# Optimization experiments

Measured on AMD Instinct MI355X. Metric: run time of the kernel, lower is better.

Reference implementation:

```python
import jax, jax.numpy as jnp
import numpy as np

B, L, D = 4, 2048, 512
H = 8
DH = D // H  # 64
SCALE = DH // H  # faithful to source: key.size(-1)//num_heads = 64//8 = 8 (multiplicative)
LN_EPS = 1e-5


def setup_inputs() -> dict:
    key = jax.random.key(0)
    ks = jax.random.split(key, 16)
    s = 1.0 / np.sqrt(D)
    inp = {
        "query": jax.random.normal(ks[0], (B, L, D), jnp.float32),
        "key": jax.random.normal(ks[1], (B, L, D), jnp.float32),
        "value": jax.random.normal(ks[2], (B, L, D), jnp.float32),
        "Wq": jax.random.uniform(ks[3], (D, D), jnp.float32, -s, s),
        "bq": jax.random.uniform(ks[4], (D,), jnp.float32, -s, s),
        "Wk": jax.random.uniform(ks[5], (D, D), jnp.float32, -s, s),
        "bk": jax.random.uniform(ks[6], (D,), jnp.float32, -s, s),
        "Wv": jax.random.uniform(ks[7], (D, D), jnp.float32, -s, s),
        "bv": jax.random.uniform(ks[8], (D,), jnp.float32, -s, s),
        "Wo": jax.random.uniform(ks[9], (D, D), jnp.float32, -s, s),
        "bo": jax.random.uniform(ks[10], (D,), jnp.float32, -s, s),
        "gamma": jnp.ones((D,), jnp.float32),
        "beta": jnp.zeros((D,), jnp.float32),
    }
    return inp


def _layer_norm(x, gamma, beta):
    mu = jnp.mean(x, axis=-1, keepdims=True)
    var = jnp.mean(jnp.square(x - mu), axis=-1, keepdims=True)
    return (x - mu) * jax.lax.rsqrt(var + LN_EPS) * gamma + beta


def reference(query, key, value, Wq, bq, Wk, bk, Wv, bv, Wo, bo, gamma, beta):
    res = query
    # QKV projections: [B, L, D]
    q = query @ Wq.T + bq
    k = key @ Wk.T + bk
    v = value @ Wv.T + bv
    # faithful to source: raw view(B*H, -1, DH) with NO transpose
    q = q.reshape(B * H, -1, DH)
    k = k.reshape(B * H, -1, DH)
    v = v.reshape(B * H, -1, DH)
    # bmm -> multiplicative scale -> softmax(dim=2) -> bmm
    attn = jnp.einsum('bqd,bkd->bqk', q, k) * SCALE  # [B*H, L, L]
    attn = jax.nn.softmax(attn, axis=2)
    ctx = jnp.einsum('bqk,bkd->bqd', attn, v)        # [B*H, L, DH]
    ctx = ctx.reshape(B, -1, DH * H)                  # [B, L, D]
    out = ctx @ Wo.T + bo
    out = _layer_norm(res + out, gamma, beta)
    return (out, attn)
```

## Files before the change

### kernel.cpp

```cpp
#include <hip/hip_runtime.h>

#define LSEQ 2048
#define DMODEL 512
#define DHD 64
#define SLAB (LSEQ*DHD)

typedef __attribute__((ext_vector_type(8))) short short8;
typedef __attribute__((ext_vector_type(4))) short short4v;
typedef __attribute__((ext_vector_type(4))) float f32x4;
typedef float f4raw __attribute__((ext_vector_type(4)));
typedef _Float16 half8 __attribute__((ext_vector_type(8)));
typedef _Float16 h4_t  __attribute__((ext_vector_type(4)));

__device__ __forceinline__ short f2bf(float x) {
    union { float f; unsigned u; } v; v.f = x;
    unsigned r = v.u + 0x7FFF + ((v.u >> 16) & 1);
    return (short)(r >> 16);
}
__device__ __forceinline__ float bf2f(short h) {
    union { float f; unsigned u; } v; v.u = ((unsigned)(unsigned short)h) << 16;
    return v.f;
}

#define GLOAD_LDS16(g, l) __builtin_amdgcn_global_load_lds( \
    (const __attribute__((address_space(1))) void*)(g),     \
    (__attribute__((address_space(3))) void*)(l), 16, 0, 0)

#define VMCNT0()  asm volatile("s_waitcnt vmcnt(0)" ::: "memory")
#define VMCNT2()  asm volatile("s_waitcnt vmcnt(2)" ::: "memory")
#define VMCNT4()  asm volatile("s_waitcnt vmcnt(4)" ::: "memory")
#define LGKM0()   asm volatile("s_waitcnt lgkmcnt(0)" ::: "memory")
#define SCHEDB()  __builtin_amdgcn_sched_barrier(0)
#define BARRIER() do { __builtin_amdgcn_s_barrier(); __builtin_amdgcn_sched_barrier(0); } while (0)

__global__ __launch_bounds__(256) void convw_kernel(
    const float* __restrict__ W0, const float* __restrict__ W1,
    const float* __restrict__ W2, const float* __restrict__ W3,
    short* __restrict__ F0, short* __restrict__ F1,
    short* __restrict__ F2, short* __restrict__ F3)
{
    const int which = blockIdx.y;
    const float* W = which==0 ? W0 : which==1 ? W1 : which==2 ? W2 : W3;
    short*       F = which==0 ? F0 : which==1 ? F1 : which==2 ? F2 : F3;

    const int g  = blockIdx.x * 256 + threadIdx.x;
    const int n  = g >> 6, kc = g & 63;
    const float* src = W + (size_t)n * 512 + kc * 8;
    float4 a0 = *(const float4*)src;
    float4 a1 = *(const float4*)(src + 4);
    float v[8] = {a0.x,a0.y,a0.z,a0.w,a1.x,a1.y,a1.z,a1.w};
    short8 h, l;
    #pragma unroll
    for (int j = 0; j < 8; ++j) { short hh = f2bf(v[j]); h[j] = hh; l[j] = f2bf(v[j] - bf2f(hh)); }

    const int nt = n >> 4, fr = n & 15, kt = kc >> 2, kg = kc & 3;
    short* dh = F + ((size_t)(nt*16 + kt) * 2) * 512 + fr*32 + kg*8;
    *(short8*)dh        = h;
    *(short8*)(dh + 512) = l;
}

template<int MODE>
__global__ __launch_bounds__(512) void proj2_kernel(
    const float* __restrict__ A0, const float* __restrict__ A1, const float* __restrict__ A2,
    const short* __restrict__ F0, const short* __restrict__ F1, const short* __restrict__ F2,
    const float* __restrict__ b0, const float* __restrict__ b1, const float* __restrict__ b2,
    float* __restrict__ Cf0, float* __restrict__ Cf1, float* __restrict__ Cf2,
    short* __restrict__ C00, short* __restrict__ C01, short* __restrict__ C02)
{
    __shared__ __align__(16) short Ah[64][40], Al[64][40];

    const int z = blockIdx.z;
    const float* A    = z==0 ? A0 : z==1 ? A1 : A2;
    const short* F    = z==0 ? F0 : z==1 ? F1 : F2;
    const float* bias = z==0 ? b0 : z==1 ? b1 : b2;
    float* Cf         = z==0 ? Cf0 : z==1 ? Cf1 : Cf2;
    short* C0         = z==0 ? C00 : z==1 ? C01 : C02;

    const int tid  = threadIdx.x;
    const int lane = tid & 63, wv = tid >> 6;
    const int fr = lane & 15, kg = lane >> 4;
    const int m0 = blockIdx.y * 64, n0 = blockIdx.x * 256;

    f32x4 acc[4][2];
    #pragma unroll
    for (int i = 0; i < 4; ++i)
        #pragma unroll
        for (int j = 0; j < 2; ++j) { f32x4 zo = {0.f,0.f,0.f,0.f}; acc[i][j] = zo; }

    const int srow = tid >> 3, sc4 = (tid & 7) << 2;

    for (int kt = 0; kt < 16; ++kt) {
        __syncthreads();
        {
            const float* ap = A + (size_t)(m0 + srow) * DMODEL + kt*32 + sc4;
            float4 a0 = *(const float4*)ap;
            float v[4] = {a0.x, a0.y, a0.z, a0.w};
            short4v h, l;
            #pragma unroll
            for (int j = 0; j < 4; ++j) { short hh = f2bf(v[j]); h[j] = hh; l[j] = f2bf(v[j] - bf2f(hh)); }
            *(short4v*)&Ah[srow][sc4] = h;
            *(short4v*)&Al[srow][sc4] = l;
        }
        __syncthreads();

        short8 ah[4], al[4];
        #pragma unroll
        for (int mf = 0; mf < 4; ++mf) {
            ah[mf] = *(short8*)&Ah[mf*16 + fr][kg*8];
            al[mf] = *(short8*)&Al[mf*16 + fr][kg*8];
        }
        #pragma unroll
        for (int nf = 0; nf < 2; ++nf) {
            const int nt = (n0 >> 4) + wv*2 + nf;
            const short* wf = F + ((size_t)(nt*16 + kt) * 2) * 512 + fr*32 + kg*8;
            short8 wh = *(const short8*)wf;
            short8 wl = *(const short8*)(wf + 512);
            #pragma unroll
            for (int mf = 0; mf < 4; ++mf) {
                acc[mf][nf] = __builtin_amdgcn_mfma_f32_16x16x32_bf16(ah[mf], wh, acc[mf][nf], 0,0,0);
                acc[mf][nf] = __builtin_amdgcn_mfma_f32_16x16x32_bf16(ah[mf], wl, acc[mf][nf], 0,0,0);
                acc[mf][nf] = __builtin_amdgcn_mfma_f32_16x16x32_bf16(al[mf], wh, acc[mf][nf], 0,0,0);
            }
        }
    }

    #pragma unroll
    for (int nf = 0; nf < 2; ++nf) {
        const int col = n0 + wv*32 + nf*16 + fr;
        const float bv = bias[col];
        #pragma unroll
        for (int mf = 0; mf < 4; ++mf) {
            #pragma unroll
            for (int r = 0; r < 4; ++r) {
                const int row = m0 + mf*16 + kg*4 + r;
                const float o = acc[mf][nf][r] + bv;
                const size_t idx = (size_t)row * DMODEL + col;
                if (MODE == 0) Cf[idx] = o;
                else           ((_Float16*)C0)[idx] = (_Float16)o;
            }
        }
    }
}

__global__ __launch_bounds__(256) void vtransf_kernel(
    const short* __restrict__ vh, short* __restrict__ vtf)
{
    __shared__ short T[64][72];
    const int tid = threadIdx.x;
    const int s  = blockIdx.y;
    const int t0 = blockIdx.x * 64;
    const size_t slab = (size_t)s * SLAB;

    {
        const int r = tid >> 2, c0 = (tid & 3) << 4;
        const short* src = vh + slab + (size_t)(t0 + r) * DHD + c0;
        short8 a = *(const short8*)src;
        short8 b = *(const short8*)(src + 8);
        *(short8*)&T[r][c0]     = a;
        *(short8*)&T[r][c0 + 8] = b;
    }
    __syncthreads();
    {
        const int kbl = tid >> 6, d = tid & 63;
        short8 o0, o1;
        #pragma unroll
        for (int j = 0; j < 8; ++j) { o0[j] = T[kbl*16 + j][d]; o1[j] = T[kbl*16 + 8 + j][d]; }
        short* dst = vtf + slab + ((size_t)((t0 >> 4) + kbl) * 64 + d) * 16;
        *(short8*)dst       = o0;
        *(short8*)(dst + 8) = o1;
    }
}

__global__ __launch_bounds__(512, 4) void attn_kernel(
    const _Float16* __restrict__ qf, const _Float16* __restrict__ kf,
    const _Float16* __restrict__ vtf,
    float* __restrict__ attn, float* __restrict__ ctx)
{
    __shared__ __align__(16) char KBuf[49152];
    __shared__ float redA[8][16];
    __shared__ float mrow[16], lirow[16];

    const int tid  = threadIdx.x;
    const int lane = tid & 63, wv = tid >> 6;
    const int fr = lane & 15, kg = lane >> 4;

    const int wg  = blockIdx.x;
    const int rem = wg & 1023;
    const int q0  = (rem >> 3) << 4;
    const int bh  = ((wg >> 10) << 3) + (rem & 7);
    const size_t slab = (size_t)bh * SLAB;

    half8 qa[2];
    #pragma unroll
    for (int ks = 0; ks < 2; ++ks)
        qa[ks] = *(const half8*)(qf + slab + (size_t)(q0 + fr) * DHD + ks*32 + kg*8);

    const int srow = lane >> 3;
    const int scb  = (lane & 7) ^ srow;

    f32x4 s[16];

    #define STAGE_K(TI, CUR) { \
        _Pragma("unroll") \
        for (int j = 0; j < 2; ++j) { \
            const int b = wv*2 + j; \
            GLOAD_LDS16(kf + slab + (size_t)((TI)*128 + b*8 + srow)*DHD + scb*8, \
                        KBuf + (CUR)*16384 + b*1024); \
        } }

    STAGE_K(0, 0);
    STAGE_K(1, 1);

    const int klo = (wv << 4) + fr;
    const int sw  = fr & 7;
    #pragma unroll
    for (int i = 0; i < 16; ++i) {
        if (i + 2 < 16) {
            SCHEDB();
            LGKM0();
            STAGE_K(i + 2, (i + 2) % 3);
        }

        if      (i <= 13) VMCNT4();
        else if (i == 14) VMCNT2();
        else              VMCNT0();

        const char* rp = KBuf + (i % 3)*16384 + (klo << 7);
        half8 kb0 = *(const half8*)(rp + ((kg ^ sw) << 4));
        half8 kb1 = *(const half8*)(rp + (((4 + kg) ^ sw) << 4));

        f32x4 a = {0.f,0.f,0.f,0.f};
        a = __builtin_amdgcn_mfma_f32_16x16x32_f16(kb0, qa[0], a, 0,0,0);
        a = __builtin_amdgcn_mfma_f32_16x16x32_f16(kb1, qa[1], a, 0,0,0);
        s[i] = a;
    }
    #undef STAGE_K

    float m;
    {
        f32x4 mx = s[0];
        #pragma unroll
        for (int i = 1; i < 16; ++i) {
            mx.x = fmaxf(mx.x, s[i].x); mx.y = fmaxf(mx.y, s[i].y);
            mx.z = fmaxf(mx.z, s[i].z); mx.w = fmaxf(mx.w, s[i].w);
        }
        m = fmaxf(fmaxf(mx.x, mx.y), fmaxf(mx.z, mx.w));
        m = fmaxf(m, __shfl_xor(m, 16));
        m = fmaxf(m, __shfl_xor(m, 32));
    }
    if (lane < 16) redA[wv][lane] = m;
    __syncthreads();
    if (tid < 16) {
        float mm = redA[0][tid];
        #pragma unroll
        for (int w = 1; w < 8; ++w) mm = fmaxf(mm, redA[w][tid]);
        mrow[tid] = mm;
    }
    __syncthreads();
    m = mrow[fr];

    const float C = 8.0f * 1.44269504089f;
    float sum = 0.f;
    #pragma unroll
    for (int i = 0; i < 16; ++i) {
        f32x4 p;
        p.x = exp2f((s[i].x - m) * C);
        p.y = exp2f((s[i].y - m) * C);
        p.z = exp2f((s[i].z - m) * C);
        p.w = exp2f((s[i].w - m) * C);
        s[i] = p;
        sum += (p.x + p.y) + (p.z + p.w);
    }
    sum += __shfl_xor(sum, 16);
    sum += __shfl_xor(sum, 32);
    if (lane < 16) redA[wv][lane] = sum;
    __syncthreads();
    if (tid < 16) {
        float l = 0.f;
        #pragma unroll
        for (int w = 0; w < 8; ++w) l += redA[w][tid];
        lirow[tid] = 1.0f / l;
    }
    __syncthreads();
    const float li = lirow[fr];

    f32x4 acc[4];
    #pragma unroll
    for (int db = 0; db < 4; ++db) { f32x4 z = {0.f,0.f,0.f,0.f}; acc[db] = z; }

    _Float16* PBh = (_Float16*)KBuf;
    const _Float16* vfb = vtf + slab;
    const int sq = tid >> 5, sc = tid & 31;
    float* abase = attn + ((size_t)bh * LSEQ + q0 + sq) * LSEQ + (sc << 2);

    int cur = 0;
    #pragma unroll
    for (int t = 0; t < 16; ++t) {
        f32x4 p = s[t];
        p.x *= li; p.y *= li; p.z *= li; p.w *= li;
        h4_t pw = { (_Float16)p.x, (_Float16)p.y, (_Float16)p.z, (_Float16)p.w };

        *(h4_t*)&PBh[(size_t)cur*2176 + fr*136 + (wv << 4) + (kg << 2)] = pw;

        const _Float16* vb = vfb + ((size_t)(t*8 + wv) << 10) + (fr << 4) + (kg << 2);
        #pragma unroll
        for (int db = 0; db < 4; ++db) {
            h4_t va = *(const h4_t*)(vb + db*256);
            acc[db] = __builtin_amdgcn_mfma_f32_16x16x16f16(va, pw, acc[db], 0,0,0);
        }

        LGKM0();
        BARRIER();

        h4_t pr = *(const h4_t*)&PBh[(size_t)cur*2176 + sq*136 + (sc << 2)];
        f4raw o = { (float)pr[0], (float)pr[1], (float)pr[2], (float)pr[3] };
        __builtin_nontemporal_store(o, (f4raw*)(abase + (size_t)t * 128));

        cur ^= 1;
    }

    __syncthreads();
    {
        float* pt = (float*)KBuf;
        #pragma unroll
        for (int db = 0; db < 4; ++db) {
            float4 o = { acc[db].x, acc[db].y, acc[db].z, acc[db].w };
            *(float4*)(pt + wv*1024 + fr*64 + db*16 + (kg << 2)) = o;
        }
    }
    __syncthreads();
    {
        float* pt = (float*)KBuf;
        const int e = tid << 1;
        const int q = e >> 6, d = e & 63;
        float2 r2 = {0.f, 0.f};
        #pragma unroll
        for (int w = 0; w < 8; ++w) {
            float2 t2 = *(float2*)(pt + w*1024 + q*64 + d);
            r2.x += t2.x; r2.y += t2.y;
        }
        *(float2*)(ctx + slab + (size_t)(q0 + q) * DHD + d) = r2;
    }
}

__global__ __launch_bounds__(128) void ln_kernel(
    const float* __restrict__ resid, const float* __restrict__ x,
    const float* __restrict__ gamma, const float* __restrict__ beta,
    float* __restrict__ out)
{
    const int row = blockIdx.x;
    const int tid = threadIdx.x;
    const size_t base = (size_t)row * DMODEL + tid*4;

    float4 v = *(const float4*)(x + base);
    float4 rq = *(const float4*)(resid + base);
    v.x += rq.x; v.y += rq.y; v.z += rq.z; v.w += rq.w;

    float s  = v.x + v.y + v.z + v.w;
    float ss = v.x*v.x + v.y*v.y + v.z*v.z + v.w*v.w;
    #pragma unroll
    for (int d = 1; d < 64; d <<= 1) { s += __shfl_xor(s, d); ss += __shfl_xor(ss, d); }

    __shared__ float red[2][2];
    const int wv = tid >> 6;
    if ((tid & 63) == 0) { red[wv][0] = s; red[wv][1] = ss; }
    __syncthreads();
    s  = red[0][0] + red[1][0];
    ss = red[0][1] + red[1][1];

    const float mu  = s * (1.0f/512.0f);
    const float var = ss * (1.0f/512.0f) - mu*mu;
    const float rs  = rsqrtf(var + 1e-5f);

    float4 g = *(const float4*)(gamma + tid*4);
    float4 b = *(const float4*)(beta + tid*4);
    float4 o;
    o.x = (v.x - mu) * rs * g.x + b.x;
    o.y = (v.y - mu) * rs * g.y + b.y;
    o.z = (v.z - mu) * rs * g.z + b.z;
    o.w = (v.w - mu) * rs * g.w + b.w;
    *(float4*)(out + base) = o;
}

extern "C" void kernel_launch(void* const* d_in, const int* in_sizes, int n_in,
                              void* d_out, int out_size, void* d_ws, size_t ws_size,
                              hipStream_t stream)
{
    const float* query = (const float*)d_in[0];
    const float* key   = (const float*)d_in[1];
    const float* value = (const float*)d_in[2];
    const float* Wq = (const float*)d_in[3];
    const float* bq = (const float*)d_in[4];
    const float* Wk = (const float*)d_in[5];
    const float* bk = (const float*)d_in[6];
    const float* Wv = (const float*)d_in[7];
    const float* bv = (const float*)d_in[8];
    const float* Wo = (const float*)d_in[9];
    const float* bo = (const float*)d_in[10];
    const float* gamma = (const float*)d_in[11];
    const float* beta  = (const float*)d_in[12];

    float* out  = (float*)d_out;
    float* attn = out + 4194304;

    const size_t NTOK = (size_t)8192 * 512;
    short* qv = (short*)d_ws;
    short* kv = qv + NTOK;
    short* vf = kv + NTOK;
    short* vtf = vf + NTOK;
    short* wfq = vtf + NTOK;
    short* wfk = wfq + 524288;
    short* wfv = wfk + 524288;
    short* wfo = wfv + 524288;
    float* obuf = (float*)d_ws;

    convw_kernel<<<dim3(128, 4), 256, 0, stream>>>(Wq, Wk, Wv, Wo, wfq, wfk, wfv, wfo);

    proj2_kernel<3><<<dim3(2, 128, 3), 512, 0, stream>>>(
        query, key, value, wfq, wfk, wfv, bq, bk, bv,
        nullptr, nullptr, nullptr, qv, kv, vf);

    vtransf_kernel<<<dim3(32, 32), 256, 0, stream>>>(vf, vtf);

    attn_kernel<<<4096, 512, 0, stream>>>((const _Float16*)qv, (const _Float16*)kv,
                                          (const _Float16*)vtf, attn, out );

    proj2_kernel<0><<<dim3(2, 128, 1), 512, 0, stream>>>(
        out , out, out, wfo, wfo, wfo, bo, bo, bo,
        obuf, obuf, obuf, nullptr, nullptr, nullptr);

    ln_kernel<<<8192, 128, 0, stream>>>(query, obuf, gamma, beta, out);
}
```

Before: 248.7 us.

## Fuse V transpose into QKV projection and LayerNorm into output projection

The QKV projection epilogue now writes V directly in the transposed tiled layout the attention kernel expects, removing the separate transpose kernel and its round trip. The output projection is rewritten so each block owns 64 full rows and applies bias, residual add and LayerNorm in its epilogue, removing the intermediate fp32 buffer and the separate LN kernel. The trade-off is that the output projection now launches only 128 blocks, giving low GPU occupancy, and the V stores become scattered 2-byte writes.

```diff
diff --git a/kernel.cpp b/kernel.cpp
--- a/kernel.cpp
+++ b/kernel.cpp
@@ -59,13 +59,11 @@
     *(short8*)(dh + 512) = l;
 }
 
-template<int MODE>
-__global__ __launch_bounds__(512) void proj2_kernel(
+__global__ __launch_bounds__(512) void projqkv_kernel(
     const float* __restrict__ A0, const float* __restrict__ A1, const float* __restrict__ A2,
     const short* __restrict__ F0, const short* __restrict__ F1, const short* __restrict__ F2,
     const float* __restrict__ b0, const float* __restrict__ b1, const float* __restrict__ b2,
-    float* __restrict__ Cf0, float* __restrict__ Cf1, float* __restrict__ Cf2,
-    short* __restrict__ C00, short* __restrict__ C01, short* __restrict__ C02)
+    short* __restrict__ qv, short* __restrict__ kv, short* __restrict__ vtf)
 {
     __shared__ __align__(16) short Ah[64][40], Al[64][40];
 
@@ -73,8 +71,6 @@
     const float* A    = z==0 ? A0 : z==1 ? A1 : A2;
     const short* F    = z==0 ? F0 : z==1 ? F1 : F2;
     const float* bias = z==0 ? b0 : z==1 ? b1 : b2;
-    float* Cf         = z==0 ? Cf0 : z==1 ? Cf1 : Cf2;
-    short* C0         = z==0 ? C00 : z==1 ? C01 : C02;
 
     const int tid  = threadIdx.x;
     const int lane = tid & 63, wv = tid >> 6;
@@ -133,41 +129,132 @@
             #pragma unroll
             for (int r = 0; r < 4; ++r) {
                 const int row = m0 + mf*16 + kg*4 + r;
-                const float o = acc[mf][nf][r] + bv;
-                const size_t idx = (size_t)row * DMODEL + col;
-                if (MODE == 0) Cf[idx] = o;
-                else           ((_Float16*)C0)[idx] = (_Float16)o;
-            }
-        }
-    }
-}
-
-__global__ __launch_bounds__(256) void vtransf_kernel(
-    const short* __restrict__ vh, short* __restrict__ vtf)
+                const _Float16 o = (_Float16)(acc[mf][nf][r] + bv);
+                if (z == 2) {
+                    const int s_ = row >> 8;
+                    const int l_ = ((row & 255) << 3) | (col >> 6);
+                    const int d_ = col & 63;
+                    ((_Float16*)vtf)[(size_t)s_*SLAB + (((l_ >> 4)*64 + d_) << 4) + (l_ & 15)] = o;
+                } else {
+                    _Float16* C = (z == 0) ? (_Float16*)qv : (_Float16*)kv;
+                    C[(size_t)row * DMODEL + col] = o;
+                }
+            }
+        }
+    }
+}
+
+__global__ __launch_bounds__(512) void proj3_kernel(
+    const float* __restrict__ A, const short* __restrict__ F,
+    const float* __restrict__ bias, const float* __restrict__ resid,
+    const float* __restrict__ gamma, const float* __restrict__ beta,
+    float* __restrict__ out)
 {
-    __shared__ short T[64][72];
-    const int tid = threadIdx.x;
-    const int s  = blockIdx.y;
-    const int t0 = blockIdx.x * 64;
-    const size_t slab = (size_t)s * SLAB;
-
-    {
-        const int r = tid >> 2, c0 = (tid & 3) << 4;
-        const short* src = vh + slab + (size_t)(t0 + r) * DHD + c0;
-        short8 a = *(const short8*)src;
-        short8 b = *(const short8*)(src + 8);
-        *(short8*)&T[r][c0]     = a;
-        *(short8*)&T[r][c0 + 8] = b;
-    }
-    __syncthreads();
-    {
-        const int kbl = tid >> 6, d = tid & 63;
-        short8 o0, o1;
-        #pragma unroll
-        for (int j = 0; j < 8; ++j) { o0[j] = T[kbl*16 + j][d]; o1[j] = T[kbl*16 + 8 + j][d]; }
-        short* dst = vtf + slab + ((size_t)((t0 >> 4) + kbl) * 64 + d) * 16;
-        *(short8*)dst       = o0;
-        *(short8*)(dst + 8) = o1;
+    __shared__ __align__(16) short Ah[64][40], Al[64][40];
+    __shared__ float redL[8][64][2];
+    __shared__ float murs[64][2];
+
+    const int tid  = threadIdx.x;
+    const int lane = tid & 63, wv = tid >> 6;
+    const int fr = lane & 15, kg = lane >> 4;
+    const int m0 = blockIdx.x * 64;
+
+    f32x4 acc[4][4];
+    #pragma unroll
+    for (int i = 0; i < 4; ++i)
+        #pragma unroll
+        for (int j = 0; j < 4; ++j) { f32x4 zo = {0.f,0.f,0.f,0.f}; acc[i][j] = zo; }
+
+    const int srow = tid >> 3, sc4 = (tid & 7) << 2;
+
+    for (int kt = 0; kt < 16; ++kt) {
+        __syncthreads();
+        {
+            const float* ap = A + (size_t)(m0 + srow) * DMODEL + kt*32 + sc4;
+            float4 a0 = *(const float4*)ap;
+            float v[4] = {a0.x, a0.y, a0.z, a0.w};
+            short4v h, l;
+            #pragma unroll
+            for (int j = 0; j < 4; ++j) { short hh = f2bf(v[j]); h[j] = hh; l[j] = f2bf(v[j] - bf2f(hh)); }
+            *(short4v*)&Ah[srow][sc4] = h;
+            *(short4v*)&Al[srow][sc4] = l;
+        }
+        __syncthreads();
+
+        short8 ah[4], al[4];
+        #pragma unroll
+        for (int mf = 0; mf < 4; ++mf) {
+            ah[mf] = *(short8*)&Ah[mf*16 + fr][kg*8];
+            al[mf] = *(short8*)&Al[mf*16 + fr][kg*8];
+        }
+        #pragma unroll
+        for (int nf = 0; nf < 4; ++nf) {
+            const int nt = wv*4 + nf;
+            const short* wf = F + ((size_t)(nt*16 + kt) * 2) * 512 + fr*32 + kg*8;
+            short8 wh = *(const short8*)wf;
+            short8 wl = *(const short8*)(wf + 512);
+            #pragma unroll
+            for (int mf = 0; mf < 4; ++mf) {
+                acc[mf][nf] = __builtin_amdgcn_mfma_f32_16x16x32_bf16(ah[mf], wh, acc[mf][nf], 0,0,0);
+                acc[mf][nf] = __builtin_amdgcn_mfma_f32_16x16x32_bf16(ah[mf], wl, acc[mf][nf], 0,0,0);
+                acc[mf][nf] = __builtin_amdgcn_mfma_f32_16x16x32_bf16(al[mf], wh, acc[mf][nf], 0,0,0);
+            }
+        }
+    }
+
+    float bv[4], gs[4], bs[4];
+    #pragma unroll
+    for (int nf = 0; nf < 4; ++nf) {
+        const int col = wv*64 + nf*16 + fr;
+        bv[nf] = bias[col]; gs[nf] = gamma[col]; bs[nf] = beta[col];
+    }
+
+    #pragma unroll
+    for (int mf = 0; mf < 4; ++mf) {
+        #pragma unroll
+        for (int r = 0; r < 4; ++r) {
+            const int row = m0 + mf*16 + kg*4 + r;
+            float s = 0.f, ss = 0.f;
+            #pragma unroll
+            for (int nf = 0; nf < 4; ++nf) {
+                const int col = wv*64 + nf*16 + fr;
+                float v = acc[mf][nf][r] + bv[nf] + resid[(size_t)row * DMODEL + col];
+                acc[mf][nf][r] = v;
+                s += v; ss += v*v;
+            }
+            #pragma unroll
+            for (int d = 1; d < 16; d <<= 1) { s += __shfl_xor(s, d); ss += __shfl_xor(ss, d); }
+            if (fr == 0) {
+                redL[wv][mf*16 + kg*4 + r][0] = s;
+                redL[wv][mf*16 + kg*4 + r][1] = ss;
+            }
+        }
+    }
+    __syncthreads();
+    if (tid < 64) {
+        float s = 0.f, ss = 0.f;
+        #pragma unroll
+        for (int w = 0; w < 8; ++w) { s += redL[w][tid][0]; ss += redL[w][tid][1]; }
+        const float mu  = s * (1.0f/512.0f);
+        const float var = ss * (1.0f/512.0f) - mu*mu;
+        murs[tid][0] = mu;
+        murs[tid][1] = rsqrtf(var + 1e-5f);
+    }
+    __syncthreads();
+
+    #pragma unroll
+    for (int mf = 0; mf < 4; ++mf) {
+        #pragma unroll
+        for (int r = 0; r < 4; ++r) {
+            const int rl = mf*16 + kg*4 + r;
+            const float mu = murs[rl][0], rs = murs[rl][1];
+            #pragma unroll
+            for (int nf = 0; nf < 4; ++nf) {
+                const int col = wv*64 + nf*16 + fr;
+                out[(size_t)(m0 + rl) * DMODEL + col] =
+                    (acc[mf][nf][r] - mu) * rs * gs[nf] + bs[nf];
+            }
+        }
     }
 }
 
@@ -341,45 +428,6 @@
         }
         *(float2*)(ctx + slab + (size_t)(q0 + q) * DHD + d) = r2;
     }
-}
-
-__global__ __launch_bounds__(128) void ln_kernel(
-    const float* __restrict__ resid, const float* __restrict__ x,
-    const float* __restrict__ gamma, const float* __restrict__ beta,
-    float* __restrict__ out)
-{
-    const int row = blockIdx.x;
-    const int tid = threadIdx.x;
-    const size_t base = (size_t)row * DMODEL + tid*4;
-
-    float4 v = *(const float4*)(x + base);
-    float4 rq = *(const float4*)(resid + base);
-    v.x += rq.x; v.y += rq.y; v.z += rq.z; v.w += rq.w;
-
-    float s  = v.x + v.y + v.z + v.w;
-    float ss = v.x*v.x + v.y*v.y + v.z*v.z + v.w*v.w;
-    #pragma unroll
-    for (int d = 1; d < 64; d <<= 1) { s += __shfl_xor(s, d); ss += __shfl_xor(ss, d); }
-
-    __shared__ float red[2][2];
-    const int wv = tid >> 6;
-    if ((tid & 63) == 0) { red[wv][0] = s; red[wv][1] = ss; }
-    __syncthreads();
-    s  = red[0][0] + red[1][0];
-    ss = red[0][1] + red[1][1];
-
-    const float mu  = s * (1.0f/512.0f);
-    const float var = ss * (1.0f/512.0f) - mu*mu;
-    const float rs  = rsqrtf(var + 1e-5f);
-
-    float4 g = *(const float4*)(gamma + tid*4);
-    float4 b = *(const float4*)(beta + tid*4);
-    float4 o;
-    o.x = (v.x - mu) * rs * g.x + b.x;
-    o.y = (v.y - mu) * rs * g.y + b.y;
-    o.z = (v.z - mu) * rs * g.z + b.z;
-    o.w = (v.w - mu) * rs * g.w + b.w;
-    *(float4*)(out + base) = o;
 }
 
 extern "C" void kernel_launch(void* const* d_in, const int* in_sizes, int n_in,
@@ -404,30 +452,21 @@
     float* attn = out + 4194304;
 
     const size_t NTOK = (size_t)8192 * 512;
-    short* qv = (short*)d_ws;
-    short* kv = qv + NTOK;
-    short* vf = kv + NTOK;
-    short* vtf = vf + NTOK;
+    short* qv  = (short*)d_ws;
+    short* kv  = qv + NTOK;
+    short* vtf = kv + NTOK;
     short* wfq = vtf + NTOK;
     short* wfk = wfq + 524288;
     short* wfv = wfk + 524288;
     short* wfo = wfv + 524288;
-    float* obuf = (float*)d_ws;
 
     convw_kernel<<<dim3(128, 4), 256, 0, stream>>>(Wq, Wk, Wv, Wo, wfq, wfk, wfv, wfo);
 
-    proj2_kernel<3><<<dim3(2, 128, 3), 512, 0, stream>>>(
-        query, key, value, wfq, wfk, wfv, bq, bk, bv,
-        nullptr, nullptr, nullptr, qv, kv, vf);
-
-    vtransf_kernel<<<dim3(32, 32), 256, 0, stream>>>(vf, vtf);
+    projqkv_kernel<<<dim3(2, 128, 3), 512, 0, stream>>>(
+        query, key, value, wfq, wfk, wfv, bq, bk, bv, qv, kv, vtf);
 
     attn_kernel<<<4096, 512, 0, stream>>>((const _Float16*)qv, (const _Float16*)kv,
                                           (const _Float16*)vtf, attn, out );
 
-    proj2_kernel<0><<<dim3(2, 128, 1), 512, 0, stream>>>(
-        out , out, out, wfo, wfo, wfo, bo, bo, bo,
-        obuf, obuf, obuf, nullptr, nullptr, nullptr);
-
-    ln_kernel<<<8192, 128, 0, stream>>>(query, obuf, gamma, beta, out);
-}
+    proj3_kernel<<<128, 512, 0, stream>>>(out , wfo, bo, query, gamma, beta, out);
+}
```

Measured after the change: 262.1 us. 5.4% more time.
